# Kernel tuning notes

Hardware: AMD Instinct MI355X
Metric: run time of the kernel (lower is better)

Reference implementation:

```python
import jax, jax.numpy as jnp
import numpy as np

NUM_FEATURES = 8
HIDDEN_DIM = 256
NUM_STABILIZERS = 2048
B, S = 128, 2048


def setup_inputs() -> dict:
    key = jax.random.key(0)
    ks = jax.random.split(key, 8)
    x = jax.random.normal(ks[0], (B, S, NUM_FEATURES), dtype=jnp.float32)
    final_mask = jax.random.randint(ks[1], (B, S), 0, 3, dtype=jnp.int64)
    # stacked per-feature Linear(1, hidden): W[f, h] = weight of proj f, b[f, h] = bias
    xav = float(np.sqrt(6.0 / (1 + HIDDEN_DIM)))  # xavier_uniform for Linear(1, H)
    W = jax.random.uniform(ks[2], (NUM_FEATURES, HIDDEN_DIM), minval=-xav, maxval=xav, dtype=jnp.float32)
    b = jnp.zeros((NUM_FEATURES, HIDDEN_DIM), dtype=jnp.float32)
    index_embed = 0.02 * jax.random.normal(ks[3], (NUM_STABILIZERS, HIDDEN_DIM), dtype=jnp.float32)
    final_on = jax.random.normal(ks[4], (HIDDEN_DIM,), dtype=jnp.float32)
    final_off = jax.random.normal(ks[5], (HIDDEN_DIM,), dtype=jnp.float32)
    gamma = jnp.ones((HIDDEN_DIM,), dtype=jnp.float32)
    beta = jnp.zeros((HIDDEN_DIM,), dtype=jnp.float32)
    return {"x": x, "final_mask": final_mask, "W": W, "b": b,
            "index_embed": index_embed, "final_on": final_on,
            "final_off": final_off, "gamma": gamma, "beta": beta}


def reference(x, final_mask, W, b, index_embed, final_on, final_off, gamma, beta):
    Bx, Sx, _ = x.shape
    # sum of per-feature Linear(1,H): single GEMM + summed bias
    h = jnp.einsum('bsf,fh->bsh', x, W) + b.sum(axis=0)  # [B,S,H]
    h = h + index_embed[:Sx][None, :, :]
    h = h + (final_mask == 1)[..., None] * final_on
    h = h + (final_mask == 2)[..., None] * final_off
    # LayerNorm over last dim, eps=1e-5 (torch default)
    mu = h.mean(axis=-1, keepdims=True)
    var = h.var(axis=-1, keepdims=True)
    h = (h - mu) * jax.lax.rsqrt(var + 1e-5)
    return h * gamma + beta
```

## Files before the change

kernel.cpp:

```cpp
#include <hip/hip_runtime.h>

#define HID 256
#define NFEAT 8
#define SLEN 2048

__global__ __launch_bounds__(256, 4) void stab_embed_ln_kernel(
    const float* __restrict__ x,
    const int*   __restrict__ mask,
    const float* __restrict__ W,
    const float* __restrict__ bias,
    const float* __restrict__ ie,
    const float* __restrict__ fon,
    const float* __restrict__ foff,
    const float* __restrict__ gamma,
    const float* __restrict__ beta,
    float* __restrict__ out,
    int ntokens)
{
    const int lane = threadIdx.x & 63;
    const int waveInBlock = threadIdx.x >> 6;
    const int wavesPerBlock = blockDim.x >> 6;
    const int gwave = blockIdx.x * wavesPerBlock + waveInBlock;
    const int nwaves = gridDim.x * wavesPerBlock;

    const int h0 = lane << 2;

    float wc[NFEAT][4];
#pragma unroll
    for (int f = 0; f < NFEAT; ++f) {
        const float4 w4 = *reinterpret_cast<const float4*>(W + f * HID + h0);
        wc[f][0] = w4.x; wc[f][1] = w4.y; wc[f][2] = w4.z; wc[f][3] = w4.w;
    }
    float bsum[4] = {0.f, 0.f, 0.f, 0.f};
#pragma unroll
    for (int f = 0; f < NFEAT; ++f) {
        const float4 b4 = *reinterpret_cast<const float4*>(bias + f * HID + h0);
        bsum[0] += b4.x; bsum[1] += b4.y; bsum[2] += b4.z; bsum[3] += b4.w;
    }
    const float4 g4   = *reinterpret_cast<const float4*>(gamma + h0);
    const float4 be4  = *reinterpret_cast<const float4*>(beta  + h0);
    const float4 on4  = *reinterpret_cast<const float4*>(fon   + h0);
    const float4 off4 = *reinterpret_cast<const float4*>(foff  + h0);
    const float gg[4]  = {g4.x,  g4.y,  g4.z,  g4.w};
    const float bb[4]  = {be4.x, be4.y, be4.z, be4.w};
    const float on[4]  = {on4.x, on4.y, on4.z, on4.w};
    const float offv[4]= {off4.x,off4.y,off4.z,off4.w};

    for (int t = gwave; t < ntokens; t += nwaves) {
        const int s = t & (SLEN - 1);

        const float4 x0 = *reinterpret_cast<const float4*>(x + (size_t)t * NFEAT);
        const float4 x1 = *reinterpret_cast<const float4*>(x + (size_t)t * NFEAT + 4);
        const float xs[NFEAT] = {x0.x, x0.y, x0.z, x0.w, x1.x, x1.y, x1.z, x1.w};

        float v[4] = {bsum[0], bsum[1], bsum[2], bsum[3]};
#pragma unroll
        for (int f = 0; f < NFEAT; ++f) {
            const float xf = xs[f];
#pragma unroll
            for (int j = 0; j < 4; ++j) v[j] = fmaf(xf, wc[f][j], v[j]);
        }

        const float4 e4 = *reinterpret_cast<const float4*>(ie + (size_t)s * HID + h0);
        v[0] += e4.x; v[1] += e4.y; v[2] += e4.z; v[3] += e4.w;

        const int m = mask[t];
        if (m == 1) {
#pragma unroll
            for (int j = 0; j < 4; ++j) v[j] += on[j];
        } else if (m == 2) {
#pragma unroll
            for (int j = 0; j < 4; ++j) v[j] += offv[j];
        }

        float s1 = v[0] + v[1] + v[2] + v[3];
        float s2 = v[0]*v[0] + v[1]*v[1] + v[2]*v[2] + v[3]*v[3];
#pragma unroll
        for (int o = 32; o > 0; o >>= 1) {
            s1 += __shfl_xor(s1, o, 64);
            s2 += __shfl_xor(s2, o, 64);
        }
        const float mu   = s1 * (1.0f / HID);
        const float var  = s2 * (1.0f / HID) - mu * mu;
        const float rstd = rsqrtf(var + 1e-5f);

        float4 o4;
        o4.x = (v[0] - mu) * rstd * gg[0] + bb[0];
        o4.y = (v[1] - mu) * rstd * gg[1] + bb[1];
        o4.z = (v[2] - mu) * rstd * gg[2] + bb[2];
        o4.w = (v[3] - mu) * rstd * gg[3] + bb[3];
        *reinterpret_cast<float4*>(out + (size_t)t * HID + h0) = o4;
    }
}

extern "C" void kernel_launch(void* const* d_in, const int* in_sizes, int n_in,
                              void* d_out, int out_size, void* d_ws, size_t ws_size,
                              hipStream_t stream) {
    const float* x     = (const float*)d_in[0];
    const int*   mask  = (const int*)  d_in[1];
    const float* W     = (const float*)d_in[2];
    const float* bias  = (const float*)d_in[3];
    const float* ie    = (const float*)d_in[4];
    const float* fon   = (const float*)d_in[5];
    const float* foff  = (const float*)d_in[6];
    const float* gamma = (const float*)d_in[7];
    const float* beta  = (const float*)d_in[8];
    float* out = (float*)d_out;

    const int ntokens = in_sizes[0] / NFEAT;

    const int block = 256;
    const int grid  = 2048;

    stab_embed_ln_kernel<<<grid, block, 0, stream>>>(
        x, mask, W, bias, ie, fon, foff, gamma, beta, out, ntokens);
}
```

Measured before the change: 339.5 us.

## Split embedding LayerNorm into precompute, per-token stats, and apply kernels

```diff
diff --git a/kernel.cpp b/kernel.cpp
--- a/kernel.cpp
+++ b/kernel.cpp
@@ -4,25 +4,94 @@
 #define NFEAT 8
 #define SLEN 2048
 
-__global__ __launch_bounds__(256, 4) void stab_embed_ln_kernel(
+__global__ __launch_bounds__(256) void p0_base_kernel(
+    const float* __restrict__ bias,
+    const float* __restrict__ ie,
+    float* __restrict__ base2,
+    int total4)
+{
+    const int idx = blockIdx.x * blockDim.x + threadIdx.x;
+    if (idx >= total4) return;
+    const int h0 = (idx & (HID / 4 - 1)) << 2;
+    float4 r = *reinterpret_cast<const float4*>(ie + (size_t)idx * 4);
+#pragma unroll
+    for (int f = 0; f < NFEAT; ++f) {
+        const float4 b4 = *reinterpret_cast<const float4*>(bias + f * HID + h0);
+        r.x += b4.x; r.y += b4.y; r.z += b4.z; r.w += b4.w;
+    }
+    *reinterpret_cast<float4*>(base2 + (size_t)idx * 4) = r;
+}
+
+__global__ __launch_bounds__(256, 4) void a_stats_kernel(
     const float* __restrict__ x,
     const int*   __restrict__ mask,
     const float* __restrict__ W,
-    const float* __restrict__ bias,
-    const float* __restrict__ ie,
+    const float* __restrict__ base2,
+    const float* __restrict__ fon,
+    const float* __restrict__ foff,
+    float2* __restrict__ musig,
+    int Bdim, int ntokens)
+{
+    const int lane  = threadIdx.x & 63;
+    const int gwave = (blockIdx.x * blockDim.x + threadIdx.x) >> 6;
+    const int s     = gwave >> 1;
+    const int b     = ((gwave & 1) << 6) + lane;
+    if (b >= Bdim) return;
+    const int t = b * SLEN + s;
+
+    const float4 x0 = *reinterpret_cast<const float4*>(x + (size_t)t * NFEAT);
+    const float4 x1 = *reinterpret_cast<const float4*>(x + (size_t)t * NFEAT + 4);
+    const float xs[NFEAT] = {x0.x, x0.y, x0.z, x0.w, x1.x, x1.y, x1.z, x1.w};
+    const int m = mask[t];
+    const float fm1 = (m == 1) ? 1.0f : 0.0f;
+    const float fm2 = (m == 2) ? 1.0f : 0.0f;
+
+    float s1 = 0.0f, s2 = 0.0f;
+    for (int h0 = 0; h0 < HID; h0 += 4) {
+        float4 acc = *reinterpret_cast<const float4*>(base2 + s * HID + h0);
+#pragma unroll
+        for (int f = 0; f < NFEAT; ++f) {
+            const float4 w4 = *reinterpret_cast<const float4*>(W + f * HID + h0);
+            acc.x = fmaf(xs[f], w4.x, acc.x);
+            acc.y = fmaf(xs[f], w4.y, acc.y);
+            acc.z = fmaf(xs[f], w4.z, acc.z);
+            acc.w = fmaf(xs[f], w4.w, acc.w);
+        }
+        const float4 on4 = *reinterpret_cast<const float4*>(fon  + h0);
+        const float4 of4 = *reinterpret_cast<const float4*>(foff + h0);
+        acc.x += fm1 * on4.x + fm2 * of4.x;
+        acc.y += fm1 * on4.y + fm2 * of4.y;
+        acc.z += fm1 * on4.z + fm2 * of4.z;
+        acc.w += fm1 * on4.w + fm2 * of4.w;
+        s1 += acc.x + acc.y + acc.z + acc.w;
+        s2 = fmaf(acc.x, acc.x, s2);
+        s2 = fmaf(acc.y, acc.y, s2);
+        s2 = fmaf(acc.z, acc.z, s2);
+        s2 = fmaf(acc.w, acc.w, s2);
+    }
+    const float mu   = s1 * (1.0f / HID);
+    const float var  = s2 * (1.0f / HID) - mu * mu;
+    const float rstd = rsqrtf(var + 1e-5f);
+    musig[t] = make_float2(mu, rstd);
+}
+
+__global__ __launch_bounds__(256, 4) void b_apply_kernel(
+    const float* __restrict__ x,
+    const int*   __restrict__ mask,
+    const float* __restrict__ W,
+    const float* __restrict__ base2,
     const float* __restrict__ fon,
     const float* __restrict__ foff,
     const float* __restrict__ gamma,
     const float* __restrict__ beta,
+    const float2* __restrict__ musig,
     float* __restrict__ out,
     int ntokens)
 {
     const int lane = threadIdx.x & 63;
-    const int waveInBlock = threadIdx.x >> 6;
     const int wavesPerBlock = blockDim.x >> 6;
-    const int gwave = blockIdx.x * wavesPerBlock + waveInBlock;
+    const int gwave = blockIdx.x * wavesPerBlock + (threadIdx.x >> 6);
     const int nwaves = gridDim.x * wavesPerBlock;
-
     const int h0 = lane << 2;
 
     float wc[NFEAT][4];
@@ -31,64 +100,40 @@
         const float4 w4 = *reinterpret_cast<const float4*>(W + f * HID + h0);
         wc[f][0] = w4.x; wc[f][1] = w4.y; wc[f][2] = w4.z; wc[f][3] = w4.w;
     }
-    float bsum[4] = {0.f, 0.f, 0.f, 0.f};
-#pragma unroll
-    for (int f = 0; f < NFEAT; ++f) {
-        const float4 b4 = *reinterpret_cast<const float4*>(bias + f * HID + h0);
-        bsum[0] += b4.x; bsum[1] += b4.y; bsum[2] += b4.z; bsum[3] += b4.w;
-    }
-    const float4 g4   = *reinterpret_cast<const float4*>(gamma + h0);
-    const float4 be4  = *reinterpret_cast<const float4*>(beta  + h0);
-    const float4 on4  = *reinterpret_cast<const float4*>(fon   + h0);
-    const float4 off4 = *reinterpret_cast<const float4*>(foff  + h0);
-    const float gg[4]  = {g4.x,  g4.y,  g4.z,  g4.w};
-    const float bb[4]  = {be4.x, be4.y, be4.z, be4.w};
-    const float on[4]  = {on4.x, on4.y, on4.z, on4.w};
-    const float offv[4]= {off4.x,off4.y,off4.z,off4.w};
+    const float4 g4  = *reinterpret_cast<const float4*>(gamma + h0);
+    const float4 be4 = *reinterpret_cast<const float4*>(beta  + h0);
 
     for (int t = gwave; t < ntokens; t += nwaves) {
         const int s = t & (SLEN - 1);
 
+        const float2 ms = musig[t];
+        float4 acc = *reinterpret_cast<const float4*>(base2 + (size_t)s * HID + h0);
         const float4 x0 = *reinterpret_cast<const float4*>(x + (size_t)t * NFEAT);
         const float4 x1 = *reinterpret_cast<const float4*>(x + (size_t)t * NFEAT + 4);
+        const int m = mask[t];
+
+        if (m == 1) {
+            const float4 on4 = *reinterpret_cast<const float4*>(fon + h0);
+            acc.x += on4.x; acc.y += on4.y; acc.z += on4.z; acc.w += on4.w;
+        } else if (m == 2) {
+            const float4 of4 = *reinterpret_cast<const float4*>(foff + h0);
+            acc.x += of4.x; acc.y += of4.y; acc.z += of4.z; acc.w += of4.w;
+        }
+
         const float xs[NFEAT] = {x0.x, x0.y, x0.z, x0.w, x1.x, x1.y, x1.z, x1.w};
-
-        float v[4] = {bsum[0], bsum[1], bsum[2], bsum[3]};
 #pragma unroll
         for (int f = 0; f < NFEAT; ++f) {
-            const float xf = xs[f];
-#pragma unroll
-            for (int j = 0; j < 4; ++j) v[j] = fmaf(xf, wc[f][j], v[j]);
+            acc.x = fmaf(xs[f], wc[f][0], acc.x);
+            acc.y = fmaf(xs[f], wc[f][1], acc.y);
+            acc.z = fmaf(xs[f], wc[f][2], acc.z);
+            acc.w = fmaf(xs[f], wc[f][3], acc.w);
         }
 
-        const float4 e4 = *reinterpret_cast<const float4*>(ie + (size_t)s * HID + h0);
-        v[0] += e4.x; v[1] += e4.y; v[2] += e4.z; v[3] += e4.w;
-
-        const int m = mask[t];
-        if (m == 1) {
-#pragma unroll
-            for (int j = 0; j < 4; ++j) v[j] += on[j];
-        } else if (m == 2) {
-#pragma unroll
-            for (int j = 0; j < 4; ++j) v[j] += offv[j];
-        }
-
-        float s1 = v[0] + v[1] + v[2] + v[3];
-        float s2 = v[0]*v[0] + v[1]*v[1] + v[2]*v[2] + v[3]*v[3];
-#pragma unroll
-        for (int o = 32; o > 0; o >>= 1) {
-            s1 += __shfl_xor(s1, o, 64);
-            s2 += __shfl_xor(s2, o, 64);
-        }
-        const float mu   = s1 * (1.0f / HID);
-        const float var  = s2 * (1.0f / HID) - mu * mu;
-        const float rstd = rsqrtf(var + 1e-5f);
-
         float4 o4;
-        o4.x = (v[0] - mu) * rstd * gg[0] + bb[0];
-        o4.y = (v[1] - mu) * rstd * gg[1] + bb[1];
-        o4.z = (v[2] - mu) * rstd * gg[2] + bb[2];
-        o4.w = (v[3] - mu) * rstd * gg[3] + bb[3];
+        o4.x = (acc.x - ms.x) * ms.y * g4.x + be4.x;
+        o4.y = (acc.y - ms.x) * ms.y * g4.y + be4.y;
+        o4.z = (acc.z - ms.x) * ms.y * g4.z + be4.z;
+        o4.w = (acc.w - ms.x) * ms.y * g4.w + be4.w;
         *reinterpret_cast<float4*>(out + (size_t)t * HID + h0) = o4;
     }
 }
@@ -108,10 +153,22 @@
     float* out = (float*)d_out;
 
     const int ntokens = in_sizes[0] / NFEAT;
+    const int Bdim    = ntokens / SLEN;
 
-    const int block = 256;
-    const int grid  = 2048;
+    float*  base2 = (float*)d_ws;
+    float2* musig = (float2*)((char*)d_ws + (size_t)SLEN * HID * sizeof(float));
 
-    stab_embed_ln_kernel<<<grid, block, 0, stream>>>(
-        x, mask, W, bias, ie, fon, foff, gamma, beta, out, ntokens);
+    {
+        const int total4 = SLEN * HID / 4;
+        p0_base_kernel<<<(total4 + 255) / 256, 256, 0, stream>>>(bias, ie, base2, total4);
+    }
+    {
+        const int waves = 2 * SLEN;
+        a_stats_kernel<<<(waves * 64) / 256, 256, 0, stream>>>(
+            x, mask, W, base2, fon, foff, musig, Bdim, ntokens);
+    }
+    {
+        b_apply_kernel<<<2048, 256, 0, stream>>>(
+            x, mask, W, base2, fon, foff, gamma, beta, musig, out, ntokens);
+    }
 }
```

After: 327.7 us. 1.04x faster.
